# Optimization experiments

Hardware: AMD Instinct MI355X
Metric: run time of the kernel (lower is better)

## Reference

```python
import jax, jax.numpy as jnp
import numpy as np

N = 20000      # nodes
E = 200000     # edges
IN = 128       # in_feat
OUT = 128      # out_feat
NB = 8         # num_bases
SI = IN // NB  # submat_in = 16
SO = OUT // NB # submat_out = 16
R = 230        # num_rels
T = 365        # total_times


def setup_inputs() -> dict:
    key = jax.random.key(0)
    ks = jax.random.split(key, 11)
    h = jax.random.normal(ks[0], (N, IN), jnp.float32)
    edge_norm = jax.random.uniform(ks[1], (E, 1), jnp.float32)
    node_norm = jax.random.uniform(ks[2], (N, 1), jnp.float32)
    weight = jax.random.normal(ks[3], (R, NB * SI * SO), jnp.float32) * 0.05
    h_bias = jnp.zeros((OUT,), jnp.float32)
    loop_weight = jax.random.normal(ks[4], (IN, OUT), jnp.float32) * 0.05
    time_embed = jax.random.normal(ks[5], (T, IN), jnp.float32) * 0.05
    edge_src = jax.random.randint(ks[6], (E,), 0, N)
    edge_dst = jax.random.randint(ks[7], (E,), 0, N)
    edge_type = jax.random.randint(ks[8], (E,), 0, R)
    time_idx = jax.random.randint(ks[9], (N,), 0, T)
    return dict(h=h, edge_norm=edge_norm, node_norm=node_norm, weight=weight,
                h_bias=h_bias, loop_weight=loop_weight, time_embed=time_embed,
                edge_src=edge_src, edge_dst=edge_dst, edge_type=edge_type,
                time_idx=time_idx)


def reference(h, edge_norm, node_norm, weight, h_bias, loop_weight, time_embed,
              edge_src, edge_dst, edge_type, time_idx):
    # self-loop message
    loop_message = h @ loop_weight                              # [N, OUT]
    # msg_func: per-edge relation weight gather + block-diagonal bmm
    W_e = weight[edge_type].reshape(-1, NB, SI, SO)             # [E, NB, SI, SO]
    src = h[edge_src].reshape(-1, NB, SI)                       # [E, NB, SI]
    msg = jnp.einsum('ebi,ebio->ebo', src, W_e).reshape(-1, OUT)  # [E, OUT]
    msg = msg * edge_norm
    # fn.sum aggregation over destination nodes
    agg = jax.ops.segment_sum(msg, edge_dst, num_segments=N)    # [N, OUT]
    # apply_func: scale by node norm, then bias + self loop + activation
    node_repr = agg * node_norm
    node_repr = node_repr + h_bias + loop_message
    node_repr = jax.nn.relu(node_repr)
    # get_time_embedding: per-node time embedding gather
    time_embedding = time_embed[time_idx]                       # [N, IN]
    return node_repr, time_embedding
```

## Files before the change

### kernel.cpp

```cpp
#include <hip/hip_runtime.h>
#include <hip/hip_bf16.h>

#define N 20000
#define E 200000
#define IN 128
#define OUT 128
#define NB 8
#define SI 16
#define SO 16
#define R 230
#define T 365

__device__ float g_agg[(size_t)N * OUT];

__global__ void zero_agg_kernel() {
    long i = (long)blockIdx.x * blockDim.x + threadIdx.x;
    long stride = (long)gridDim.x * blockDim.x;
    for (; i < (long)N * OUT; i += stride) g_agg[i] = 0.f;
}

__global__ void edge_kernel(const float* __restrict__ h,
                            const float* __restrict__ edge_norm,
                            const float* __restrict__ weight,
                            const int* __restrict__ edge_src,
                            const int* __restrict__ edge_dst,
                            const int* __restrict__ edge_type) {
    long idx = (long)blockIdx.x * blockDim.x + threadIdx.x;
    int e = (int)(idx >> 7);
    if (e >= E) return;
    int o  = (int)(idx & 127);
    int b  = o >> 4;
    int ol = o & 15;
    int s = edge_src[e];
    int d = edge_dst[e];
    int r = edge_type[e];
    const float* src = h + (long)s * IN + b * SI;
    const float* W   = weight + (long)r * (NB * SI * SO) + b * (SI * SO) + ol;
    float acc = 0.f;
#pragma unroll
    for (int i = 0; i < SI; ++i)
        acc = fmaf(src[i], W[i * SO], acc);
    acc *= edge_norm[e];
    atomicAdd(&g_agg[(long)d * OUT + o], acc);
}

__global__ __launch_bounds__(128) void node_kernel(
        const float* __restrict__ h,
        const float* __restrict__ node_norm,
        const float* __restrict__ h_bias,
        const float* __restrict__ loop_weight,
        const float* __restrict__ time_embed,
        const int* __restrict__ time_idx,
        float* __restrict__ out) {
    __shared__ float hsm[IN * 16];
    const int tid  = threadIdx.x;
    const int base = blockIdx.x * 16;

    for (int k = tid; k < 16 * IN; k += 128) {
        int nl = k >> 7;
        int i  = k & 127;
        hsm[i * 16 + nl] = h[(long)(base + nl) * IN + i];
    }
    __syncthreads();

    float acc[16];
#pragma unroll
    for (int nl = 0; nl < 16; ++nl) acc[nl] = 0.f;

    for (int i = 0; i < IN; ++i) {
        float w = loop_weight[(long)i * OUT + tid];
        const float4* hp = reinterpret_cast<const float4*>(&hsm[i * 16]);
#pragma unroll
        for (int q = 0; q < 4; ++q) {
            float4 hv = hp[q];
            acc[q * 4 + 0] = fmaf(hv.x, w, acc[q * 4 + 0]);
            acc[q * 4 + 1] = fmaf(hv.y, w, acc[q * 4 + 1]);
            acc[q * 4 + 2] = fmaf(hv.z, w, acc[q * 4 + 2]);
            acc[q * 4 + 3] = fmaf(hv.w, w, acc[q * 4 + 3]);
        }
    }

    float bias = h_bias[tid];
#pragma unroll
    for (int nl = 0; nl < 16; ++nl) {
        int n = base + nl;
        float v = g_agg[(long)n * OUT + tid] * node_norm[n] + bias + acc[nl];
        out[(long)n * OUT + tid] = fmaxf(v, 0.f);
        out[(long)N * OUT + (long)n * IN + tid] =
            time_embed[(long)time_idx[n] * IN + tid];
    }
}

extern "C" void kernel_launch(void* const* d_in, const int* in_sizes, int n_in,
                              void* d_out, int out_size, void* d_ws, size_t ws_size,
                              hipStream_t stream) {
    const float* h           = (const float*)d_in[0];
    const float* edge_norm   = (const float*)d_in[1];
    const float* node_norm   = (const float*)d_in[2];
    const float* weight      = (const float*)d_in[3];
    const float* h_bias      = (const float*)d_in[4];
    const float* loop_weight = (const float*)d_in[5];
    const float* time_embed  = (const float*)d_in[6];
    const int*   edge_src    = (const int*)d_in[7];
    const int*   edge_dst    = (const int*)d_in[8];
    const int*   edge_type   = (const int*)d_in[9];
    const int*   time_idx    = (const int*)d_in[10];
    float* out = (float*)d_out;

    zero_agg_kernel<<<2560, 256, 0, stream>>>();

    const long total = (long)E * 128;
    const int  bs = 256;
    edge_kernel<<<(int)((total + bs - 1) / bs), bs, 0, stream>>>(
        h, edge_norm, weight, edge_src, edge_dst, edge_type);

    node_kernel<<<N / 16, 128, 0, stream>>>(
        h, node_norm, h_bias, loop_weight, time_embed, time_idx, out);
}
```

Baseline: 239.9 us.

## Replace atomic scatter-add with CSR-by-destination gather fused into node kernel

Builds a destination-sorted edge list (histogram, single-block scan, atomic scatter) each call, then computes per-edge messages inside the node kernel by walking each node's incoming edges and accumulating in registers. This removes the 25.6M float atomics into a global aggregate buffer and the zeroing pass. In exchange it adds four small preprocessing kernels, including a serial-ish one-block scan, and lowers nodes per block to 4, which reduces loop_weight reuse in the self-loop matmul. Per-node edge counts vary, so wave load is uneven.

```diff
diff --git a/kernel.cpp b/kernel.cpp
--- a/kernel.cpp
+++ b/kernel.cpp
@@ -1,5 +1,4 @@
 #include <hip/hip_runtime.h>
-#include <hip/hip_bf16.h>
 
 #define N 20000
 #define E 200000
@@ -11,80 +10,147 @@
 #define R 230
 #define T 365
 
-__device__ float g_agg[(size_t)N * OUT];
+#define NPB 4
 
-__global__ void zero_agg_kernel() {
-    long i = (long)blockIdx.x * blockDim.x + threadIdx.x;
-    long stride = (long)gridDim.x * blockDim.x;
-    for (; i < (long)N * OUT; i += stride) g_agg[i] = 0.f;
+__device__ int g_cnt[N];
+__device__ int g_off[N];
+__device__ int g_cur[N];
+__device__ int g_eid[E];
+
+__global__ void zero_cnt_kernel() {
+    int i = blockIdx.x * blockDim.x + threadIdx.x;
+    if (i < N) g_cnt[i] = 0;
 }
 
-__global__ void edge_kernel(const float* __restrict__ h,
-                            const float* __restrict__ edge_norm,
-                            const float* __restrict__ weight,
-                            const int* __restrict__ edge_src,
-                            const int* __restrict__ edge_dst,
-                            const int* __restrict__ edge_type) {
-    long idx = (long)blockIdx.x * blockDim.x + threadIdx.x;
-    int e = (int)(idx >> 7);
-    if (e >= E) return;
-    int o  = (int)(idx & 127);
-    int b  = o >> 4;
-    int ol = o & 15;
-    int s = edge_src[e];
-    int d = edge_dst[e];
-    int r = edge_type[e];
-    const float* src = h + (long)s * IN + b * SI;
-    const float* W   = weight + (long)r * (NB * SI * SO) + b * (SI * SO) + ol;
-    float acc = 0.f;
-#pragma unroll
-    for (int i = 0; i < SI; ++i)
-        acc = fmaf(src[i], W[i * SO], acc);
-    acc *= edge_norm[e];
-    atomicAdd(&g_agg[(long)d * OUT + o], acc);
+__global__ void hist_kernel(const int* __restrict__ edge_dst) {
+    int e = blockIdx.x * blockDim.x + threadIdx.x;
+    if (e < E) atomicAdd(&g_cnt[edge_dst[e]], 1);
 }
 
-__global__ __launch_bounds__(128) void node_kernel(
+__global__ __launch_bounds__(1024) void scan_kernel() {
+    __shared__ int part[1024];
+    const int tid = threadIdx.x;
+    const int CH = (N + 1023) / 1024;
+    const int base = tid * CH;
+    int sum = 0;
+    for (int j = 0; j < CH; ++j) {
+        int idx = base + j;
+        if (idx < N) sum += g_cnt[idx];
+    }
+    part[tid] = sum;
+    __syncthreads();
+    for (int d = 1; d < 1024; d <<= 1) {
+        int v = 0;
+        if (tid >= d) v = part[tid - d];
+        __syncthreads();
+        if (tid >= d) part[tid] += v;
+        __syncthreads();
+    }
+    int run = (tid > 0) ? part[tid - 1] : 0;
+    for (int j = 0; j < CH; ++j) {
+        int idx = base + j;
+        if (idx < N) {
+            g_off[idx] = run;
+            g_cur[idx] = run;
+            run += g_cnt[idx];
+        }
+    }
+}
+
+__global__ void scatter_kernel(const int* __restrict__ edge_dst) {
+    int e = blockIdx.x * blockDim.x + threadIdx.x;
+    if (e < E) {
+        int d = edge_dst[e];
+        int pos = atomicAdd(&g_cur[d], 1);
+        g_eid[pos] = e;
+    }
+}
+
+__global__ __launch_bounds__(128) void fused_kernel(
         const float* __restrict__ h,
+        const float* __restrict__ edge_norm,
         const float* __restrict__ node_norm,
+        const float* __restrict__ weight,
         const float* __restrict__ h_bias,
         const float* __restrict__ loop_weight,
         const float* __restrict__ time_embed,
+        const int* __restrict__ edge_src,
+        const int* __restrict__ edge_type,
         const int* __restrict__ time_idx,
         float* __restrict__ out) {
-    __shared__ float hsm[IN * 16];
+    __shared__ float hsm[IN * NPB];
     const int tid  = threadIdx.x;
-    const int base = blockIdx.x * 16;
+    const int base = blockIdx.x * NPB;
 
-    for (int k = tid; k < 16 * IN; k += 128) {
+    for (int k = tid; k < NPB * IN; k += 128) {
         int nl = k >> 7;
         int i  = k & 127;
-        hsm[i * 16 + nl] = h[(long)(base + nl) * IN + i];
+        hsm[i * NPB + nl] = h[(long)(base + nl) * IN + i];
     }
     __syncthreads();
 
-    float acc[16];
+    float acc[NPB];
 #pragma unroll
-    for (int nl = 0; nl < 16; ++nl) acc[nl] = 0.f;
+    for (int nl = 0; nl < NPB; ++nl) acc[nl] = 0.f;
 
     for (int i = 0; i < IN; ++i) {
         float w = loop_weight[(long)i * OUT + tid];
-        const float4* hp = reinterpret_cast<const float4*>(&hsm[i * 16]);
-#pragma unroll
-        for (int q = 0; q < 4; ++q) {
-            float4 hv = hp[q];
-            acc[q * 4 + 0] = fmaf(hv.x, w, acc[q * 4 + 0]);
-            acc[q * 4 + 1] = fmaf(hv.y, w, acc[q * 4 + 1]);
-            acc[q * 4 + 2] = fmaf(hv.z, w, acc[q * 4 + 2]);
-            acc[q * 4 + 3] = fmaf(hv.w, w, acc[q * 4 + 3]);
-        }
+        float4 hv = *reinterpret_cast<const float4*>(&hsm[i * NPB]);
+        acc[0] = fmaf(hv.x, w, acc[0]);
+        acc[1] = fmaf(hv.y, w, acc[1]);
+        acc[2] = fmaf(hv.z, w, acc[2]);
+        acc[3] = fmaf(hv.w, w, acc[3]);
     }
 
-    float bias = h_bias[tid];
-#pragma unroll
-    for (int nl = 0; nl < 16; ++nl) {
-        int n = base + nl;
-        float v = g_agg[(long)n * OUT + tid] * node_norm[n] + bias + acc[nl];
+    const int b  = tid >> 4;
+    const int ol = tid & 15;
+    const float bias = h_bias[tid];
+
+    for (int nl = 0; nl < NPB; ++nl) {
+        const int n   = base + nl;
+        const int st  = g_off[n];
+        const int cnt = g_cnt[n];
+        float agg = 0.f;
+        if (cnt > 0) {
+            int   s  = edge_src[g_eid[st]];
+            int   r  = edge_type[g_eid[st]];
+            float en = edge_norm[g_eid[st]];
+            for (int k = 0; k < cnt; ++k) {
+                int s2 = 0, r2 = 0;
+                float en2 = 0.f;
+                if (k + 1 < cnt) {
+                    int e2 = g_eid[st + k + 1];
+                    s2  = edge_src[e2];
+                    r2  = edge_type[e2];
+                    en2 = edge_norm[e2];
+                }
+                const float4* hp =
+                    reinterpret_cast<const float4*>(h + (long)s * IN + b * SI);
+                const float* W =
+                    weight + (long)r * (NB * SI * SO) + b * (SI * SO) + ol;
+                float4 h0 = hp[0], h1 = hp[1], h2 = hp[2], h3 = hp[3];
+                float m0 = 0.f, m1 = 0.f;
+                m0 = fmaf(h0.x, W[0 * SO],  m0);
+                m0 = fmaf(h0.y, W[1 * SO],  m0);
+                m0 = fmaf(h0.z, W[2 * SO],  m0);
+                m0 = fmaf(h0.w, W[3 * SO],  m0);
+                m1 = fmaf(h1.x, W[4 * SO],  m1);
+                m1 = fmaf(h1.y, W[5 * SO],  m1);
+                m1 = fmaf(h1.z, W[6 * SO],  m1);
+                m1 = fmaf(h1.w, W[7 * SO],  m1);
+                m0 = fmaf(h2.x, W[8 * SO],  m0);
+                m0 = fmaf(h2.y, W[9 * SO],  m0);
+                m0 = fmaf(h2.z, W[10 * SO], m0);
+                m0 = fmaf(h2.w, W[11 * SO], m0);
+                m1 = fmaf(h3.x, W[12 * SO], m1);
+                m1 = fmaf(h3.y, W[13 * SO], m1);
+                m1 = fmaf(h3.z, W[14 * SO], m1);
+                m1 = fmaf(h3.w, W[15 * SO], m1);
+                agg = fmaf(en, m0 + m1, agg);
+                s = s2; r = r2; en = en2;
+            }
+        }
+        float v = agg * node_norm[n] + bias + acc[nl];
         out[(long)n * OUT + tid] = fmaxf(v, 0.f);
         out[(long)N * OUT + (long)n * IN + tid] =
             time_embed[(long)time_idx[n] * IN + tid];
@@ -107,13 +173,11 @@
     const int*   time_idx    = (const int*)d_in[10];
     float* out = (float*)d_out;
 
-    zero_agg_kernel<<<2560, 256, 0, stream>>>();
-
-    const long total = (long)E * 128;
-    const int  bs = 256;
-    edge_kernel<<<(int)((total + bs - 1) / bs), bs, 0, stream>>>(
-        h, edge_norm, weight, edge_src, edge_dst, edge_type);
-
-    node_kernel<<<N / 16, 128, 0, stream>>>(
-        h, node_norm, h_bias, loop_weight, time_embed, time_idx, out);
+    zero_cnt_kernel<<<(N + 255) / 256, 256, 0, stream>>>();
+    hist_kernel<<<(E + 255) / 256, 256, 0, stream>>>(edge_dst);
+    scan_kernel<<<1, 1024, 0, stream>>>();
+    scatter_kernel<<<(E + 255) / 256, 256, 0, stream>>>(edge_dst);
+    fused_kernel<<<N / NPB, 128, 0, stream>>>(
+        h, edge_norm, node_norm, weight, h_bias, loop_weight,
+        time_embed, edge_src, edge_type, time_idx, out);
 }
```

New measurement: 270.2 us. +12.6%, slower.

## Replace atomic edge scatter with CSR-by-destination gather aggregation

Applied to the files above, without the earlier changes.

Builds a per-destination edge list each call (histogram, atomic offset allocation, scatter) and aggregates messages per node in one block, replacing 25.6M float atomics with plain stores. The relation weights are pre-transposed so each thread reads contiguous float4 rows. The node kernel is also widened to 32 nodes per 256-thread block with padded shared memory. This adds several small launches and integer atomics, and the edge order within a node is nondeterministic, so summation order varies between runs.

```diff
diff --git a/kernel.cpp b/kernel.cpp
--- a/kernel.cpp
+++ b/kernel.cpp
@@ -1,5 +1,4 @@
 #include <hip/hip_runtime.h>
-#include <hip/hip_bf16.h>
 
 #define N 20000
 #define E 200000
@@ -11,83 +10,161 @@
 #define R 230
 #define T 365
 
+__device__ float g_W_t[(size_t)R * NB * SO * SI];
 __device__ float g_agg[(size_t)N * OUT];
+__device__ int   g_cnt[N];
+__device__ int   g_off[N];
+__device__ int   g_cur[N];
+__device__ int   g_eid[E];
+__device__ int   g_total;
 
-__global__ void zero_agg_kernel() {
-    long i = (long)blockIdx.x * blockDim.x + threadIdx.x;
-    long stride = (long)gridDim.x * blockDim.x;
-    for (; i < (long)N * OUT; i += stride) g_agg[i] = 0.f;
+__global__ void prep_kernel(const float* __restrict__ weight) {
+    int t = blockIdx.x * blockDim.x + threadIdx.x;
+    if (t < R * NB * SO * SI) {
+        int r  = t >> 11;
+        int b  = (t >> 8) & 7;
+        int ol = (t >> 4) & 15;
+        int i  = t & 15;
+        g_W_t[t] = weight[(long)r * 2048 + b * 256 + i * 16 + ol];
+    }
+    if (t < N) g_cnt[t] = 0;
+    if (t == 0) g_total = 0;
 }
 
-__global__ void edge_kernel(const float* __restrict__ h,
-                            const float* __restrict__ edge_norm,
-                            const float* __restrict__ weight,
-                            const int* __restrict__ edge_src,
-                            const int* __restrict__ edge_dst,
-                            const int* __restrict__ edge_type) {
-    long idx = (long)blockIdx.x * blockDim.x + threadIdx.x;
-    int e = (int)(idx >> 7);
-    if (e >= E) return;
-    int o  = (int)(idx & 127);
-    int b  = o >> 4;
-    int ol = o & 15;
-    int s = edge_src[e];
-    int d = edge_dst[e];
-    int r = edge_type[e];
-    const float* src = h + (long)s * IN + b * SI;
-    const float* W   = weight + (long)r * (NB * SI * SO) + b * (SI * SO) + ol;
-    float acc = 0.f;
-#pragma unroll
-    for (int i = 0; i < SI; ++i)
-        acc = fmaf(src[i], W[i * SO], acc);
-    acc *= edge_norm[e];
-    atomicAdd(&g_agg[(long)d * OUT + o], acc);
+__global__ void hist_kernel(const int* __restrict__ edge_dst) {
+    int e = blockIdx.x * blockDim.x + threadIdx.x;
+    if (e < E) atomicAdd(&g_cnt[edge_dst[e]], 1);
 }
 
-__global__ __launch_bounds__(128) void node_kernel(
+__global__ void alloc_kernel() {
+    int n = blockIdx.x * blockDim.x + threadIdx.x;
+    if (n < N) {
+        int c = g_cnt[n];
+        int off = atomicAdd(&g_total, c);
+        g_off[n] = off;
+        g_cur[n] = off;
+    }
+}
+
+__global__ void scatter_kernel(const int* __restrict__ edge_dst) {
+    int e = blockIdx.x * blockDim.x + threadIdx.x;
+    if (e < E) {
+        int pos = atomicAdd(&g_cur[edge_dst[e]], 1);
+        g_eid[pos] = e;
+    }
+}
+
+__global__ __launch_bounds__(256) void agg_kernel(
         const float* __restrict__ h,
+        const float* __restrict__ edge_norm,
         const float* __restrict__ node_norm,
+        const int* __restrict__ edge_src,
+        const int* __restrict__ edge_type) {
+    __shared__ float part[128];
+    const int n    = blockIdx.x;
+    const int tid  = threadIdx.x;
+    const int slot = tid >> 7;
+    const int o    = tid & 127;
+    const int b    = o >> 4;
+    const int ol   = o & 15;
+
+    const int st  = g_off[n];
+    const int cnt = g_cnt[n];
+
+    float agg = 0.f;
+    int k = slot;
+    if (k < cnt) {
+        int e0 = g_eid[st + k];
+        int   s  = edge_src[e0];
+        int   r  = edge_type[e0];
+        float en = edge_norm[e0];
+        while (k < cnt) {
+            int k2 = k + 2;
+            int s2 = 0, r2 = 0;
+            float en2 = 0.f;
+            if (k2 < cnt) {
+                int e2 = g_eid[st + k2];
+                s2  = edge_src[e2];
+                r2  = edge_type[e2];
+                en2 = edge_norm[e2];
+            }
+            const float4* hp =
+                reinterpret_cast<const float4*>(h + (long)s * IN + b * SI);
+            const float4* wp = reinterpret_cast<const float4*>(
+                g_W_t + (long)r * 2048 + b * 256 + ol * 16);
+            float4 h0 = hp[0], h1 = hp[1], h2 = hp[2], h3 = hp[3];
+            float4 w0 = wp[0], w1 = wp[1], w2 = wp[2], w3 = wp[3];
+            float m0 = 0.f, m1 = 0.f;
+            m0 = fmaf(h0.x, w0.x, m0); m0 = fmaf(h0.y, w0.y, m0);
+            m0 = fmaf(h0.z, w0.z, m0); m0 = fmaf(h0.w, w0.w, m0);
+            m1 = fmaf(h1.x, w1.x, m1); m1 = fmaf(h1.y, w1.y, m1);
+            m1 = fmaf(h1.z, w1.z, m1); m1 = fmaf(h1.w, w1.w, m1);
+            m0 = fmaf(h2.x, w2.x, m0); m0 = fmaf(h2.y, w2.y, m0);
+            m0 = fmaf(h2.z, w2.z, m0); m0 = fmaf(h2.w, w2.w, m0);
+            m1 = fmaf(h3.x, w3.x, m1); m1 = fmaf(h3.y, w3.y, m1);
+            m1 = fmaf(h3.z, w3.z, m1); m1 = fmaf(h3.w, w3.w, m1);
+            agg = fmaf(en, m0 + m1, agg);
+            s = s2; r = r2; en = en2; k = k2;
+        }
+    }
+    if (slot == 1) part[o] = agg;
+    __syncthreads();
+    if (slot == 0) {
+        float a = agg + part[o];
+        g_agg[(long)n * OUT + o] = a * node_norm[n];
+    }
+}
+
+__global__ __launch_bounds__(256) void node_kernel(
+        const float* __restrict__ h,
         const float* __restrict__ h_bias,
         const float* __restrict__ loop_weight,
         const float* __restrict__ time_embed,
         const int* __restrict__ time_idx,
         float* __restrict__ out) {
-    __shared__ float hsm[IN * 16];
+    __shared__ float hsm[IN * 36];
     const int tid  = threadIdx.x;
-    const int base = blockIdx.x * 16;
+    const int half = tid >> 7;
+    const int o    = tid & 127;
+    const int base = blockIdx.x * 32;
 
-    for (int k = tid; k < 16 * IN; k += 128) {
+    for (int k = tid; k < 32 * IN; k += 256) {
         int nl = k >> 7;
         int i  = k & 127;
-        hsm[i * 16 + nl] = h[(long)(base + nl) * IN + i];
+        hsm[i * 36 + nl] = h[(long)(base + nl) * IN + i];
     }
     __syncthreads();
 
     float acc[16];
 #pragma unroll
-    for (int nl = 0; nl < 16; ++nl) acc[nl] = 0.f;
+    for (int q = 0; q < 16; ++q) acc[q] = 0.f;
 
+#pragma unroll 4
     for (int i = 0; i < IN; ++i) {
-        float w = loop_weight[(long)i * OUT + tid];
-        const float4* hp = reinterpret_cast<const float4*>(&hsm[i * 16]);
-#pragma unroll
-        for (int q = 0; q < 4; ++q) {
-            float4 hv = hp[q];
-            acc[q * 4 + 0] = fmaf(hv.x, w, acc[q * 4 + 0]);
-            acc[q * 4 + 1] = fmaf(hv.y, w, acc[q * 4 + 1]);
-            acc[q * 4 + 2] = fmaf(hv.z, w, acc[q * 4 + 2]);
-            acc[q * 4 + 3] = fmaf(hv.w, w, acc[q * 4 + 3]);
-        }
+        float w = loop_weight[(long)i * OUT + o];
+        const float* row = &hsm[i * 36 + half * 16];
+        float4 a0 = *reinterpret_cast<const float4*>(row + 0);
+        float4 a1 = *reinterpret_cast<const float4*>(row + 4);
+        float4 a2 = *reinterpret_cast<const float4*>(row + 8);
+        float4 a3 = *reinterpret_cast<const float4*>(row + 12);
+        acc[0]  = fmaf(a0.x, w, acc[0]);  acc[1]  = fmaf(a0.y, w, acc[1]);
+        acc[2]  = fmaf(a0.z, w, acc[2]);  acc[3]  = fmaf(a0.w, w, acc[3]);
+        acc[4]  = fmaf(a1.x, w, acc[4]);  acc[5]  = fmaf(a1.y, w, acc[5]);
+        acc[6]  = fmaf(a1.z, w, acc[6]);  acc[7]  = fmaf(a1.w, w, acc[7]);
+        acc[8]  = fmaf(a2.x, w, acc[8]);  acc[9]  = fmaf(a2.y, w, acc[9]);
+        acc[10] = fmaf(a2.z, w, acc[10]); acc[11] = fmaf(a2.w, w, acc[11]);
+        acc[12] = fmaf(a3.x, w, acc[12]); acc[13] = fmaf(a3.y, w, acc[13]);
+        acc[14] = fmaf(a3.z, w, acc[14]); acc[15] = fmaf(a3.w, w, acc[15]);
     }
 
-    float bias = h_bias[tid];
+    const float bias = h_bias[o];
 #pragma unroll
-    for (int nl = 0; nl < 16; ++nl) {
-        int n = base + nl;
-        float v = g_agg[(long)n * OUT + tid] * node_norm[n] + bias + acc[nl];
-        out[(long)n * OUT + tid] = fmaxf(v, 0.f);
-        out[(long)N * OUT + (long)n * IN + tid] =
-            time_embed[(long)time_idx[n] * IN + tid];
+    for (int q = 0; q < 16; ++q) {
+        int n = base + half * 16 + q;
+        float v = g_agg[(long)n * OUT + o] + bias + acc[q];
+        out[(long)n * OUT + o] = fmaxf(v, 0.f);
+        out[(long)N * OUT + (long)n * IN + o] =
+            time_embed[(long)time_idx[n] * IN + o];
     }
 }
 
@@ -107,13 +184,12 @@
     const int*   time_idx    = (const int*)d_in[10];
     float* out = (float*)d_out;
 
-    zero_agg_kernel<<<2560, 256, 0, stream>>>();
-
-    const long total = (long)E * 128;
-    const int  bs = 256;
-    edge_kernel<<<(int)((total + bs - 1) / bs), bs, 0, stream>>>(
-        h, edge_norm, weight, edge_src, edge_dst, edge_type);
-
-    node_kernel<<<N / 16, 128, 0, stream>>>(
-        h, node_norm, h_bias, loop_weight, time_embed, time_idx, out);
+    prep_kernel<<<(R * NB * SO * SI + 255) / 256, 256, 0, stream>>>(weight);
+    hist_kernel<<<(E + 255) / 256, 256, 0, stream>>>(edge_dst);
+    alloc_kernel<<<(N + 255) / 256, 256, 0, stream>>>();
+    scatter_kernel<<<(E + 255) / 256, 256, 0, stream>>>(edge_dst);
+    agg_kernel<<<N, 256, 0, stream>>>(h, edge_norm, node_norm,
+                                      edge_src, edge_type);
+    node_kernel<<<N / 32, 256, 0, stream>>>(h, h_bias, loop_weight,
+                                            time_embed, time_idx, out);
 }
```

New measurement: 287.9 us. 20.0% more time.

## Replace atomic scatter with relation-sorted message pass and CSR gather reduction

Applied to the files above, without the earlier changes.

Drops the zero-fill and the per-element float atomics into the aggregation buffer. Edges are now counted by destination and by relation, bucketed into CSR-style offsets, and processed in relation-sorted order so each thread reuses its transposed weight row across consecutive edges. Messages go into a per-edge staging buffer at their destination slot, and the node kernel gathers and sums each node's messages before adding the self-loop. This writes and rereads a large E×OUT intermediate and adds several small launches with integer atomics in exchange for removing contended float atomics.

```diff
diff --git a/kernel.cpp b/kernel.cpp
--- a/kernel.cpp
+++ b/kernel.cpp
@@ -1,5 +1,4 @@
 #include <hip/hip_runtime.h>
-#include <hip/hip_bf16.h>
 
 #define N 20000
 #define E 200000
@@ -11,37 +10,159 @@
 #define R 230
 #define T 365
 
-__device__ float g_agg[(size_t)N * OUT];
-
-__global__ void zero_agg_kernel() {
-    long i = (long)blockIdx.x * blockDim.x + threadIdx.x;
-    long stride = (long)gridDim.x * blockDim.x;
-    for (; i < (long)N * OUT; i += stride) g_agg[i] = 0.f;
-}
-
-__global__ void edge_kernel(const float* __restrict__ h,
-                            const float* __restrict__ edge_norm,
-                            const float* __restrict__ weight,
-                            const int* __restrict__ edge_src,
-                            const int* __restrict__ edge_dst,
-                            const int* __restrict__ edge_type) {
-    long idx = (long)blockIdx.x * blockDim.x + threadIdx.x;
-    int e = (int)(idx >> 7);
-    if (e >= E) return;
-    int o  = (int)(idx & 127);
-    int b  = o >> 4;
-    int ol = o & 15;
-    int s = edge_src[e];
-    int d = edge_dst[e];
-    int r = edge_type[e];
-    const float* src = h + (long)s * IN + b * SI;
-    const float* W   = weight + (long)r * (NB * SI * SO) + b * (SI * SO) + ol;
-    float acc = 0.f;
-#pragma unroll
-    for (int i = 0; i < SI; ++i)
-        acc = fmaf(src[i], W[i * SO], acc);
-    acc *= edge_norm[e];
-    atomicAdd(&g_agg[(long)d * OUT + o], acc);
+__device__ float g_W_t[(size_t)R * NB * SO * SI];
+__device__ float g_msg[(size_t)E * OUT];
+__device__ int   g_cnt_d[N];
+__device__ int   g_off_d[N];
+__device__ int   g_cur_d[N];
+__device__ int   g_cnt_r[R * 16];
+__device__ int   g_cur_r[R * 16];
+__device__ int   g_pos[E];
+__device__ int   g_eid_r[E];
+__device__ int   g_total_d;
+__device__ int   g_total_r;
+
+__global__ void prep_kernel(const float* __restrict__ weight) {
+    int t = blockIdx.x * blockDim.x + threadIdx.x;
+    if (t < R * NB * SO * SI) {
+        int r  = t >> 11;
+        int b  = (t >> 8) & 7;
+        int ol = (t >> 4) & 15;
+        int i  = t & 15;
+        g_W_t[t] = weight[(long)r * 2048 + b * 256 + i * 16 + ol];
+    }
+    if (t < N) g_cnt_d[t] = 0;
+    if (t < R * 16) g_cnt_r[t] = 0;
+    if (t == 0) { g_total_d = 0; g_total_r = 0; }
+}
+
+__global__ __launch_bounds__(256) void hist_kernel(
+        const int* __restrict__ edge_dst,
+        const int* __restrict__ edge_type) {
+    __shared__ int lh[R];
+    for (int j = threadIdx.x; j < R; j += 256) lh[j] = 0;
+    __syncthreads();
+    for (long e = (long)blockIdx.x * blockDim.x + threadIdx.x; e < E;
+         e += (long)gridDim.x * blockDim.x) {
+        atomicAdd(&g_cnt_d[edge_dst[e]], 1);
+        atomicAdd(&lh[edge_type[e]], 1);
+    }
+    __syncthreads();
+    for (int j = threadIdx.x; j < R; j += 256)
+        if (lh[j]) atomicAdd(&g_cnt_r[j * 16], lh[j]);
+}
+
+__global__ __launch_bounds__(256) void alloc_kernel() {
+    int idx  = blockIdx.x * blockDim.x + threadIdx.x;
+    int lane = threadIdx.x & 63;
+    const int NPAD = 20032;
+    if (idx < NPAD) {
+        int c = (idx < N) ? g_cnt_d[idx] : 0;
+        int x = c;
+        for (int d = 1; d < 64; d <<= 1) {
+            int y = __shfl_up(x, d);
+            if (lane >= d) x += y;
+        }
+        int base = 0;
+        if (lane == 63) base = atomicAdd(&g_total_d, x);
+        base = __shfl(base, 63);
+        if (idx < N) {
+            int off = base + x - c;
+            g_off_d[idx] = off;
+            g_cur_d[idx] = off;
+        }
+    } else if (idx < NPAD + 256) {
+        int j = idx - NPAD;
+        int c = (j < R) ? g_cnt_r[j * 16] : 0;
+        int x = c;
+        for (int d = 1; d < 64; d <<= 1) {
+            int y = __shfl_up(x, d);
+            if (lane >= d) x += y;
+        }
+        int base = 0;
+        if (lane == 63) base = atomicAdd(&g_total_r, x);
+        base = __shfl(base, 63);
+        if (j < R) g_cur_r[j * 16] = base + x - c;
+    }
+}
+
+__global__ void scatter_kernel(const int* __restrict__ edge_dst,
+                               const int* __restrict__ edge_type) {
+    int e = blockIdx.x * blockDim.x + threadIdx.x;
+    if (e < E) {
+        g_pos[e] = atomicAdd(&g_cur_d[edge_dst[e]], 1);
+        int pr = atomicAdd(&g_cur_r[edge_type[e] * 16], 1);
+        g_eid_r[pr] = e;
+    }
+}
+
+__global__ __launch_bounds__(256) void msg_kernel(
+        const float* __restrict__ h,
+        const float* __restrict__ edge_norm,
+        const int* __restrict__ edge_src,
+        const int* __restrict__ edge_type) {
+    const int tid = threadIdx.x;
+    const int grp = tid >> 7;
+    const int o   = tid & 127;
+    const int b   = o >> 4;
+    const int ol  = o & 15;
+
+    int lo = blockIdx.x * 128 + grp * 64;
+    int hi = lo + 64; if (hi > E) hi = E;
+    if (lo >= hi) return;
+
+    int rcur = -1;
+    float4 w0, w1, w2, w3;
+
+    int   e0 = g_eid_r[lo];
+    int   s0 = edge_src[e0];
+    int   r0 = edge_type[e0];
+    float n0 = edge_norm[e0];
+    int   p0 = g_pos[e0];
+    const float4* hp = reinterpret_cast<const float4*>(h + (long)s0 * IN + b * SI);
+    float4 hA0 = hp[0], hA1 = hp[1], hA2 = hp[2], hA3 = hp[3];
+
+    int s1 = 0, r1 = 0, p1 = 0; float n1 = 0.f;
+    if (lo + 1 < hi) {
+        int e1 = g_eid_r[lo + 1];
+        s1 = edge_src[e1]; r1 = edge_type[e1];
+        n1 = edge_norm[e1]; p1 = g_pos[e1];
+    }
+
+    for (int k = lo; k < hi; ++k) {
+        int s2 = 0, r2 = 0, p2 = 0; float n2 = 0.f;
+        if (k + 2 < hi) {
+            int e2 = g_eid_r[k + 2];
+            s2 = edge_src[e2]; r2 = edge_type[e2];
+            n2 = edge_norm[e2]; p2 = g_pos[e2];
+        }
+        float4 hB0, hB1, hB2, hB3;
+        if (k + 1 < hi) {
+            const float4* hq =
+                reinterpret_cast<const float4*>(h + (long)s1 * IN + b * SI);
+            hB0 = hq[0]; hB1 = hq[1]; hB2 = hq[2]; hB3 = hq[3];
+        }
+        if (r0 != rcur) {
+            const float4* wp = reinterpret_cast<const float4*>(
+                g_W_t + (long)r0 * 2048 + b * 256 + ol * 16);
+            w0 = wp[0]; w1 = wp[1]; w2 = wp[2]; w3 = wp[3];
+            rcur = r0;
+        }
+        float m0 = 0.f, m1 = 0.f;
+        m0 = fmaf(hA0.x, w0.x, m0); m0 = fmaf(hA0.y, w0.y, m0);
+        m0 = fmaf(hA0.z, w0.z, m0); m0 = fmaf(hA0.w, w0.w, m0);
+        m1 = fmaf(hA1.x, w1.x, m1); m1 = fmaf(hA1.y, w1.y, m1);
+        m1 = fmaf(hA1.z, w1.z, m1); m1 = fmaf(hA1.w, w1.w, m1);
+        m0 = fmaf(hA2.x, w2.x, m0); m0 = fmaf(hA2.y, w2.y, m0);
+        m0 = fmaf(hA2.z, w2.z, m0); m0 = fmaf(hA2.w, w2.w, m0);
+        m1 = fmaf(hA3.x, w3.x, m1); m1 = fmaf(hA3.y, w3.y, m1);
+        m1 = fmaf(hA3.z, w3.z, m1); m1 = fmaf(hA3.w, w3.w, m1);
+        g_msg[(long)p0 * OUT + o] = n0 * (m0 + m1);
+
+        hA0 = hB0; hA1 = hB1; hA2 = hB2; hA3 = hB3;
+        s0 = s1; r0 = r1; n0 = n1; p0 = p1;
+        s1 = s2; r1 = r2; n1 = n2; p1 = p2;
+    }
 }
 
 __global__ __launch_bounds__(128) void node_kernel(
@@ -52,42 +173,62 @@
         const float* __restrict__ time_embed,
         const int* __restrict__ time_idx,
         float* __restrict__ out) {
-    __shared__ float hsm[IN * 16];
-    const int tid  = threadIdx.x;
-    const int base = blockIdx.x * 16;
-
-    for (int k = tid; k < 16 * IN; k += 128) {
+    __shared__ float hsm[IN * 8];
+    const int o    = threadIdx.x;
+    const int base = blockIdx.x * 8;
+
+    for (int k = o; k < 8 * IN; k += 128) {
         int nl = k >> 7;
         int i  = k & 127;
-        hsm[i * 16 + nl] = h[(long)(base + nl) * IN + i];
+        hsm[i * 8 + nl] = h[(long)(base + nl) * IN + i];
     }
     __syncthreads();
 
-    float acc[16];
-#pragma unroll
-    for (int nl = 0; nl < 16; ++nl) acc[nl] = 0.f;
-
-    for (int i = 0; i < IN; ++i) {
-        float w = loop_weight[(long)i * OUT + tid];
-        const float4* hp = reinterpret_cast<const float4*>(&hsm[i * 16]);
-#pragma unroll
-        for (int q = 0; q < 4; ++q) {
-            float4 hv = hp[q];
-            acc[q * 4 + 0] = fmaf(hv.x, w, acc[q * 4 + 0]);
-            acc[q * 4 + 1] = fmaf(hv.y, w, acc[q * 4 + 1]);
-            acc[q * 4 + 2] = fmaf(hv.z, w, acc[q * 4 + 2]);
-            acc[q * 4 + 3] = fmaf(hv.w, w, acc[q * 4 + 3]);
-        }
-    }
-
-    float bias = h_bias[tid];
-#pragma unroll
-    for (int nl = 0; nl < 16; ++nl) {
+    float acc[8];
+#pragma unroll
+    for (int nl = 0; nl < 8; ++nl) {
+        int n  = base + nl;
+        int st = g_off_d[n];
+        int cn = g_cnt_d[n];
+        float a0 = 0.f, a1 = 0.f;
+        int k = 0;
+        for (; k + 1 < cn; k += 2) {
+            a0 += g_msg[(long)(st + k) * OUT + o];
+            a1 += g_msg[(long)(st + k + 1) * OUT + o];
+        }
+        if (k < cn) a0 += g_msg[(long)(st + k) * OUT + o];
+        acc[nl] = (a0 + a1) * node_norm[n];
+    }
+
+    float sl[8];
+#pragma unroll
+    for (int nl = 0; nl < 8; ++nl) sl[nl] = 0.f;
+
+    for (int i0 = 0; i0 < IN; i0 += 8) {
+        float w[8];
+#pragma unroll
+        for (int j = 0; j < 8; ++j)
+            w[j] = loop_weight[(long)(i0 + j) * OUT + o];
+#pragma unroll
+        for (int j = 0; j < 8; ++j) {
+            const float* row = &hsm[(i0 + j) * 8];
+            float4 p0 = *reinterpret_cast<const float4*>(row);
+            float4 p1 = *reinterpret_cast<const float4*>(row + 4);
+            sl[0] = fmaf(p0.x, w[j], sl[0]); sl[1] = fmaf(p0.y, w[j], sl[1]);
+            sl[2] = fmaf(p0.z, w[j], sl[2]); sl[3] = fmaf(p0.w, w[j], sl[3]);
+            sl[4] = fmaf(p1.x, w[j], sl[4]); sl[5] = fmaf(p1.y, w[j], sl[5]);
+            sl[6] = fmaf(p1.z, w[j], sl[6]); sl[7] = fmaf(p1.w, w[j], sl[7]);
+        }
+    }
+
+    const float bias = h_bias[o];
+#pragma unroll
+    for (int nl = 0; nl < 8; ++nl) {
         int n = base + nl;
-        float v = g_agg[(long)n * OUT + tid] * node_norm[n] + bias + acc[nl];
-        out[(long)n * OUT + tid] = fmaxf(v, 0.f);
-        out[(long)N * OUT + (long)n * IN + tid] =
-            time_embed[(long)time_idx[n] * IN + tid];
+        float v = acc[nl] + bias + sl[nl];
+        out[(long)n * OUT + o] = fmaxf(v, 0.f);
+        out[(long)N * OUT + (long)n * IN + o] =
+            time_embed[(long)time_idx[n] * IN + o];
     }
 }
 
@@ -107,13 +248,12 @@
     const int*   time_idx    = (const int*)d_in[10];
     float* out = (float*)d_out;
 
-    zero_agg_kernel<<<2560, 256, 0, stream>>>();
-
-    const long total = (long)E * 128;
-    const int  bs = 256;
-    edge_kernel<<<(int)((total + bs - 1) / bs), bs, 0, stream>>>(
-        h, edge_norm, weight, edge_src, edge_dst, edge_type);
-
-    node_kernel<<<N / 16, 128, 0, stream>>>(
-        h, node_norm, h_bias, loop_weight, time_embed, time_idx, out);
-}
+    prep_kernel<<<(R * NB * SO * SI + 255) / 256, 256, 0, stream>>>(weight);
+    hist_kernel<<<200, 256, 0, stream>>>(edge_dst, edge_type);
+    alloc_kernel<<<(20032 + 256 + 255) / 256, 256, 0, stream>>>();
+    scatter_kernel<<<(E + 255) / 256, 256, 0, stream>>>(edge_dst, edge_type);
+    msg_kernel<<<(E + 127) / 128, 256, 0, stream>>>(h, edge_norm,
+                                                    edge_src, edge_type);
+    node_kernel<<<N / 8, 128, 0, stream>>>(h, node_norm, h_bias, loop_weight,
+                                           time_embed, time_idx, out);
+}
```

Measured after the change: 300.9 us. 1.25x slower.
